# Performance work log

Measured on AMD Instinct MI355X. Metric: run time of the kernel, lower is better.

The kernel has to match this reference:

```python
import jax, jax.numpy as jnp
import numpy as np


def _igd(x, pf):
    # pf: [M, d] reference front, x: [N, d] candidate set
    # squared Euclidean distances via ||a||^2 + ||b||^2 - 2 a.b (cdist expansion)
    pf_sq = jnp.sum(pf * pf, axis=1, keepdims=True)          # [M, 1]
    x_sq = jnp.sum(x * x, axis=1, keepdims=True).T            # [1, N]
    cross = pf @ x.T                                          # [M, N]
    d2 = jnp.maximum(pf_sq + x_sq - 2.0 * cross, 0.0)
    dist = jnp.sqrt(d2)                                       # [M, N]
    # IGD: mean over reference points of min distance to candidate set
    return jnp.mean(jnp.min(dist, axis=1))


def setup_inputs() -> dict:
    key = jax.random.key(0)
    k1, k2 = jax.random.split(key)
    N, M, D = 16384, 16384, 64
    x = jax.random.normal(k1, (N, D), dtype=jnp.float32)
    pf = jax.random.normal(k2, (M, D), dtype=jnp.float32)
    return {"x": x, "pf": pf}


def reference(x, pf):
    return _igd(x, pf)
```

## Files before the change

kernel.cpp:

```cpp
#include <hip/hip_runtime.h>


typedef float f32x16 __attribute__((ext_vector_type(16)));
typedef int i32x8 __attribute__((ext_vector_type(8)));
typedef unsigned long long u64;

#define DIM 64
#define NSPLIT 12
#define UNITB 2048
#define CHUNKU 8
#define CHUNKB (CHUNKU * UNITB)
#define MTILE 256

union BFrag { u64 q[4]; i32x8 v; };

__device__ inline unsigned char enc_e4m3(float f) {
    unsigned int u = __float_as_uint(f);
    unsigned int s = (u >> 24) & 0x80u;
    unsigned int a = u & 0x7FFFFFFFu;
    if ((a >> 23) >= 121u) {
        unsigned int lsb = (a >> 20) & 1u;
        unsigned int r = a + 0x7FFFFu + lsb;
        int e = (int)(r >> 23) - 120;
        unsigned int m = (r >> 20) & 7u;
        if (e > 15 || (e == 15 && m == 7u)) return (unsigned char)(s | 0x7Eu);
        return (unsigned char)(s | ((unsigned)e << 3) | m);
    }
    int m = (int)rintf(__uint_as_float(a) * 512.0f);
    return (unsigned char)(s | (unsigned)m);
}

__device__ inline float dec_e4m3(unsigned char b) {
    int e = (b >> 3) & 15, m = b & 7;
    float v = e ? __uint_as_float((unsigned)((e + 120) << 23) | ((unsigned)m << 20))
                : (float)m * 0.001953125f;
    return (b & 0x80) ? -v : v;
}

__global__ void pack_kernel(const float* __restrict__ x, const float* __restrict__ pf,
                            unsigned char* __restrict__ Bp, unsigned char* __restrict__ Ab,
                            float* __restrict__ xsq, float* __restrict__ pfsq,
                            float* __restrict__ out, int N, int M) {
    int gid = blockIdx.x * blockDim.x + threadIdx.x;
    if (gid == 0) out[0] = 0.f;
    if (gid < N * 4) {
        int col = gid >> 2, t = gid & 3;
        const float* s = x + (size_t)col * DIM + t * 16;
        float partial = 0.f;
        u64 w[2] = {0, 0};
#pragma unroll
        for (int h = 0; h < 2; ++h) {
            float4 v0 = *(const float4*)(s + h * 8);
            float4 v1 = *(const float4*)(s + h * 8 + 4);
            float f[8] = {v0.x, v0.y, v0.z, v0.w, v1.x, v1.y, v1.z, v1.w};
#pragma unroll
            for (int j = 0; j < 8; ++j) {
                unsigned char b = enc_e4m3(f[j]);
                w[h] |= (u64)b << (8 * j);
                float d = dec_e4m3(b);
                partial += d * d;
            }
        }
        int u = col >> 5, c31 = col & 31;
        unsigned char* ub = Bp + (size_t)u * UNITB;
        int h = t >> 1;
#pragma unroll
        for (int ss = 0; ss < 2; ++ss) {
            int q = (t & 1) * 2 + ss;
            *(u64*)(ub + (size_t)q * 512 + (size_t)(h * 32 + c31) * 8) = w[ss];
        }
        partial += __shfl_xor(partial, 1);
        partial += __shfl_xor(partial, 2);
        if (t == 0) xsq[col] = partial;
    } else {
        int g = gid - N * 4;
        int row = g >> 2, q = g & 3;
        if (row >= M) return;
        const float* s = pf + (size_t)row * DIM + q * 16;
        float partial = 0.f;
        u64 w[2] = {0, 0};
#pragma unroll
        for (int h = 0; h < 2; ++h) {
            float4 v0 = *(const float4*)(s + h * 8);
            float4 v1 = *(const float4*)(s + h * 8 + 4);
            float f[8] = {v0.x, v0.y, v0.z, v0.w, v1.x, v1.y, v1.z, v1.w};
#pragma unroll
            for (int j = 0; j < 8; ++j) {
                unsigned char b = enc_e4m3(f[j] * -2.f);
                w[h] |= (u64)b << (8 * j);
                float d = dec_e4m3(b);
                partial += d * d;
            }
        }
        *(u64*)(Ab + (size_t)row * DIM + q * 16)     = w[0];
        *(u64*)(Ab + (size_t)row * DIM + q * 16 + 8) = w[1];
        partial += __shfl_xor(partial, 1);
        partial += __shfl_xor(partial, 2);
        if (q == 0) pfsq[row] = partial * 0.25f;
    }
}

__global__ __launch_bounds__(256, 3)
void igd_main(const unsigned char* __restrict__ A, const unsigned char* __restrict__ Bp,
              const float* __restrict__ xsq, float* __restrict__ partial, int N) {
    __shared__ unsigned char ldsB[2][CHUNKB];
    __shared__ float ldsX[2][CHUNKU * 32];
    const int tid = threadIdx.x;
    const int mTile  = blockIdx.x;
    const int nsplit = blockIdx.y;
    const int lane = tid & 63;
    const int wave = tid >> 6;
    const int half = lane >> 5;
    const int l31  = lane & 31;
    const int rowBase = mTile * MTILE + wave * 64;

    const int utotal = N / 32;
    const int ubase  = utotal / NSPLIT;
    const int urem   = utotal % NSPLIT;
    const int ustart = nsplit * ubase + (nsplit < urem ? nsplit : urem);
    const int ucount = ubase + (nsplit < urem ? 1 : 0);
    const int nch = (ucount + CHUNKU - 1) / CHUNKU;

    BFrag a[2];
#pragma unroll
    for (int g = 0; g < 2; ++g) {
        const unsigned char* ap = A + (size_t)(rowBase + 32 * g + l31) * DIM + half * 32;
#pragma unroll
        for (int qq = 0; qq < 4; ++qq)
            a[g].q[qq] = *(const u64*)(ap + qq * 8);
    }

    const unsigned char* gB = Bp + (size_t)ustart * UNITB;
    const float* gX = xsq + ustart * 32;

#define STAGE(c, buf)                                                          \
    {                                                                          \
        int bytes = (ucount - (c) * CHUNKU) < CHUNKU ? (ucount - (c) * CHUNKU) * UNITB : CHUNKB; \
        const unsigned char* src = gB + (size_t)(c) * CHUNKB;                  \
        _Pragma("unroll")                                                      \
        for (int i = 0; i < 4; ++i) {                                          \
            int off = i * 4096 + tid * 16;                                     \
            if (off < bytes)                                                   \
                *(float4*)(&ldsB[buf][off]) = *(const float4*)(src + off);     \
        }                                                                      \
        int xcnt = bytes >> 6;                                                 \
        if (tid < xcnt) ldsX[buf][tid] = gX[(c) * (CHUNKU * 32) + tid];        \
    }

    f32x16 zero, m0, m1;
#pragma unroll
    for (int r = 0; r < 16; ++r) { zero[r] = 0.f; m0[r] = 1e30f; m1[r] = 1e30f; }

    BFrag b0, b1;

#define LOADF(rr, lb, u)                                                       \
    {                                                                          \
        const unsigned char* p = (lb) + (u) * UNITB;                           \
        rr.q[0] = *(const u64*)(p);                                            \
        rr.q[1] = *(const u64*)(p + 512);                                      \
        rr.q[2] = *(const u64*)(p + 1024);                                     \
        rr.q[3] = *(const u64*)(p + 1536);                                     \
    }

#define COMPUTE(rr, xq)                                                        \
    {                                                                          \
        f32x16 acc0 = __builtin_amdgcn_mfma_scale_f32_32x32x64_f8f6f4(         \
            a[0].v, rr.v, zero, 0, 0, 0, 0x7F7F7F7F, 0, 0x7F7F7F7F);           \
        f32x16 acc1 = __builtin_amdgcn_mfma_scale_f32_32x32x64_f8f6f4(         \
            a[1].v, rr.v, zero, 0, 0, 0, 0x7F7F7F7F, 0, 0x7F7F7F7F);           \
        _Pragma("unroll")                                                      \
        for (int r = 0; r < 16; ++r) {                                         \
            m0[r] = fminf(m0[r], acc0[r] + (xq));                              \
            m1[r] = fminf(m1[r], acc1[r] + (xq));                              \
        }                                                                      \
    }

    STAGE(0, 0);
    __syncthreads();

    for (int c = 0; c < nch; ++c) {
        const int buf = c & 1;
        if (c + 1 < nch) STAGE(c + 1, buf ^ 1);
        const int cnt = (ucount - c * CHUNKU) < CHUNKU ? (ucount - c * CHUNKU) : CHUNKU;
        const unsigned char* lb = &ldsB[buf][0] + lane * 8;
        const float* lx = &ldsX[buf][0] + l31;
        if (cnt == CHUNKU) {
            LOADF(b0, lb, 0);
#pragma unroll
            for (int u = 0; u < CHUNKU; u += 2) {
                LOADF(b1, lb, u + 1);
                COMPUTE(b0, lx[u * 32]);
                if (u + 2 < CHUNKU) LOADF(b0, lb, u + 2);
                COMPUTE(b1, lx[(u + 1) * 32]);
            }
        } else {
            for (int u = 0; u < cnt; ++u) {
                LOADF(b0, lb, u);
                COMPUTE(b0, lx[u * 32]);
            }
        }
        __syncthreads();
    }
#undef STAGE
#undef LOADF
#undef COMPUTE

#pragma unroll
    for (int mask = 1; mask <= 16; mask <<= 1) {
#pragma unroll
        for (int r = 0; r < 16; ++r) {
            m0[r] = fminf(m0[r], __shfl_xor(m0[r], mask));
            m1[r] = fminf(m1[r], __shfl_xor(m1[r], mask));
        }
    }
    if (l31 == 0) {
#pragma unroll
        for (int r = 0; r < 16; ++r) {
            int row0 = rowBase + (r & 3) + 8 * (r >> 2) + 4 * half;
            partial[(size_t)row0 * NSPLIT + nsplit] = m0[r];
            partial[(size_t)(row0 + 32) * NSPLIT + nsplit] = m1[r];
        }
    }
}

__global__ void reduce_kernel(const float* __restrict__ partial, const float* __restrict__ pfsq,
                              float* __restrict__ out, int M, float invM) {
    int row = blockIdx.x * blockDim.x + threadIdx.x;
    float v = 0.f;
    if (row < M) {
        const float* p = partial + (size_t)row * NSPLIT;
        float mn = 3.4e38f;
#pragma unroll
        for (int s = 0; s < NSPLIT; ++s) mn = fminf(mn, p[s]);
        float d2 = mn + pfsq[row];
        v = sqrtf(fmaxf(d2, 0.f)) * invM;
    }
#pragma unroll
    for (int m = 1; m < 64; m <<= 1) v += __shfl_xor(v, m);
    __shared__ float wsum[4];
    int lane = threadIdx.x & 63, w = threadIdx.x >> 6;
    if (lane == 0) wsum[w] = v;
    __syncthreads();
    if (threadIdx.x == 0) atomicAdd(out, wsum[0] + wsum[1] + wsum[2] + wsum[3]);
}

extern "C" void kernel_launch(void* const* d_in, const int* in_sizes, int n_in,
                              void* d_out, int out_size, void* d_ws, size_t ws_size,
                              hipStream_t stream) {
    const float* x  = (const float*)d_in[0];
    const float* pf = (const float*)d_in[1];
    const int N = in_sizes[0] / DIM;
    const int M = in_sizes[1] / DIM;

    char* ws = (char*)d_ws;
    unsigned char* Bp = (unsigned char*)ws;
    unsigned char* Ab = (unsigned char*)(ws + (size_t)N * DIM);
    float* xsq  = (float*)(ws + (size_t)(N + M) * DIM);
    float* pfsq = xsq + N;
    float* part = pfsq + M;

    int packThreads = (N + M) * 4;
    pack_kernel<<<dim3((packThreads + 255) / 256), 256, 0, stream>>>(
        x, pf, Bp, Ab, xsq, pfsq, (float*)d_out, N, M);
    igd_main<<<dim3(M / MTILE, NSPLIT), 256, 0, stream>>>(Ab, Bp, xsq, part, N);
    reduce_kernel<<<dim3((M + 255) / 256), 256, 0, stream>>>(part, pfsq, (float*)d_out, M, 1.f / (float)M);
}
```

Baseline: 92.31 us.

## Load whole per-block B slice into LDS via direct global-to-LDS loads

Doubles the N-split so each block handles at most 22 units, then loads its entire B slice and x-norms into LDS at once with global_load_lds. This replaces the double-buffered chunk loop and its per-chunk barriers with a single barrier and a flat compute loop. It adds grid blocks and partial-min traffic for the reduce kernel. The larger LDS footprint (~45KB) may limit occupancy, and the global-load latency is no longer overlapped with compute inside a block.

```diff
diff --git a/kernel.cpp b/kernel.cpp
--- a/kernel.cpp
+++ b/kernel.cpp
@@ -6,13 +6,23 @@
 typedef unsigned long long u64;
 
 #define DIM 64
-#define NSPLIT 12
+#define NSPLIT 24
 #define UNITB 2048
-#define CHUNKU 8
-#define CHUNKB (CHUNKU * UNITB)
+#define MAXU 22
 #define MTILE 256
 
 union BFrag { u64 q[4]; i32x8 v; };
+
+__device__ __forceinline__ void g2lds16(const void* g, void* l) {
+    __builtin_amdgcn_global_load_lds(
+        (const __attribute__((address_space(1))) unsigned int*)g,
+        (__attribute__((address_space(3))) unsigned int*)l, 16, 0, 0);
+}
+__device__ __forceinline__ void g2lds4(const void* g, void* l) {
+    __builtin_amdgcn_global_load_lds(
+        (const __attribute__((address_space(1))) unsigned int*)g,
+        (__attribute__((address_space(3))) unsigned int*)l, 4, 0, 0);
+}
 
 __device__ inline unsigned char enc_e4m3(float f) {
     unsigned int u = __float_as_uint(f);
@@ -103,8 +113,8 @@
 __global__ __launch_bounds__(256, 3)
 void igd_main(const unsigned char* __restrict__ A, const unsigned char* __restrict__ Bp,
               const float* __restrict__ xsq, float* __restrict__ partial, int N) {
-    __shared__ unsigned char ldsB[2][CHUNKB];
-    __shared__ float ldsX[2][CHUNKU * 32];
+    __shared__ unsigned char ldsB[MAXU * UNITB];
+    __shared__ float ldsX[MAXU * 32];
     const int tid = threadIdx.x;
     const int mTile  = blockIdx.x;
     const int nsplit = blockIdx.y;
@@ -119,7 +129,24 @@
     const int urem   = utotal % NSPLIT;
     const int ustart = nsplit * ubase + (nsplit < urem ? nsplit : urem);
     const int ucount = ubase + (nsplit < urem ? 1 : 0);
-    const int nch = (ucount + CHUNKU - 1) / CHUNKU;
+
+    const unsigned char* gB = Bp + (size_t)ustart * UNITB;
+    const float* gX = xsq + ustart * 32;
+
+    {
+        int bytes = ucount * UNITB;
+#pragma unroll
+        for (int i = 0; i < 11; ++i) {
+            int off = i * 4096 + tid * 16;
+            if (off < bytes) g2lds16(gB + off, &ldsB[off]);
+        }
+        int xcnt = ucount * 32;
+#pragma unroll
+        for (int j = 0; j < 3; ++j) {
+            int idx = j * 256 + tid;
+            if (idx < xcnt) g2lds4(gX + idx, &ldsX[idx]);
+        }
+    }
 
     BFrag a[2];
 #pragma unroll
@@ -130,44 +157,27 @@
             a[g].q[qq] = *(const u64*)(ap + qq * 8);
     }
 
-    const unsigned char* gB = Bp + (size_t)ustart * UNITB;
-    const float* gX = xsq + ustart * 32;
-
-#define STAGE(c, buf)                                                          \
+    f32x16 zero, m0, m1;
+#pragma unroll
+    for (int r = 0; r < 16; ++r) { zero[r] = 0.f; m0[r] = 1e30f; m1[r] = 1e30f; }
+
+    __syncthreads();
+
+#define LOADF(rr, u)                                                           \
     {                                                                          \
-        int bytes = (ucount - (c) * CHUNKU) < CHUNKU ? (ucount - (c) * CHUNKU) * UNITB : CHUNKB; \
-        const unsigned char* src = gB + (size_t)(c) * CHUNKB;                  \
-        _Pragma("unroll")                                                      \
-        for (int i = 0; i < 4; ++i) {                                          \
-            int off = i * 4096 + tid * 16;                                     \
-            if (off < bytes)                                                   \
-                *(float4*)(&ldsB[buf][off]) = *(const float4*)(src + off);     \
-        }                                                                      \
-        int xcnt = bytes >> 6;                                                 \
-        if (tid < xcnt) ldsX[buf][tid] = gX[(c) * (CHUNKU * 32) + tid];        \
-    }
-
-    f32x16 zero, m0, m1;
-#pragma unroll
-    for (int r = 0; r < 16; ++r) { zero[r] = 0.f; m0[r] = 1e30f; m1[r] = 1e30f; }
-
-    BFrag b0, b1;
-
-#define LOADF(rr, lb, u)                                                       \
-    {                                                                          \
-        const unsigned char* p = (lb) + (u) * UNITB;                           \
+        const unsigned char* p = &ldsB[0] + lane * 8 + (u) * UNITB;            \
         rr.q[0] = *(const u64*)(p);                                            \
         rr.q[1] = *(const u64*)(p + 512);                                      \
         rr.q[2] = *(const u64*)(p + 1024);                                     \
         rr.q[3] = *(const u64*)(p + 1536);                                     \
     }
 
-#define COMPUTE(rr, xq)                                                        \
+#define STEP(bfrag, xq)                                                        \
     {                                                                          \
         f32x16 acc0 = __builtin_amdgcn_mfma_scale_f32_32x32x64_f8f6f4(         \
-            a[0].v, rr.v, zero, 0, 0, 0, 0x7F7F7F7F, 0, 0x7F7F7F7F);           \
+            a[0].v, bfrag.v, zero, 0, 0, 0, 0x7F7F7F7F, 0, 0x7F7F7F7F);        \
         f32x16 acc1 = __builtin_amdgcn_mfma_scale_f32_32x32x64_f8f6f4(         \
-            a[1].v, rr.v, zero, 0, 0, 0, 0x7F7F7F7F, 0, 0x7F7F7F7F);           \
+            a[1].v, bfrag.v, zero, 0, 0, 0, 0x7F7F7F7F, 0, 0x7F7F7F7F);        \
         _Pragma("unroll")                                                      \
         for (int r = 0; r < 16; ++r) {                                         \
             m0[r] = fminf(m0[r], acc0[r] + (xq));                              \
@@ -175,35 +185,18 @@
         }                                                                      \
     }
 
-    STAGE(0, 0);
-    __syncthreads();
-
-    for (int c = 0; c < nch; ++c) {
-        const int buf = c & 1;
-        if (c + 1 < nch) STAGE(c + 1, buf ^ 1);
-        const int cnt = (ucount - c * CHUNKU) < CHUNKU ? (ucount - c * CHUNKU) : CHUNKU;
-        const unsigned char* lb = &ldsB[buf][0] + lane * 8;
-        const float* lx = &ldsX[buf][0] + l31;
-        if (cnt == CHUNKU) {
-            LOADF(b0, lb, 0);
-#pragma unroll
-            for (int u = 0; u < CHUNKU; u += 2) {
-                LOADF(b1, lb, u + 1);
-                COMPUTE(b0, lx[u * 32]);
-                if (u + 2 < CHUNKU) LOADF(b0, lb, u + 2);
-                COMPUTE(b1, lx[(u + 1) * 32]);
-            }
-        } else {
-            for (int u = 0; u < cnt; ++u) {
-                LOADF(b0, lb, u);
-                COMPUTE(b0, lx[u * 32]);
-            }
-        }
-        __syncthreads();
-    }
-#undef STAGE
+    {
+        BFrag b0, b1;
+        LOADF(b0, 0);
+        for (int u = 0; u < ucount; u += 2) {
+            if (u + 1 < ucount) LOADF(b1, u + 1);
+            STEP(b0, ldsX[u * 32 + l31]);
+            if (u + 2 < ucount) LOADF(b0, u + 2);
+            if (u + 1 < ucount) STEP(b1, ldsX[(u + 1) * 32 + l31]);
+        }
+    }
 #undef LOADF
-#undef COMPUTE
+#undef STEP
 
 #pragma unroll
     for (int mask = 1; mask <= 16; mask <<= 1) {
@@ -230,7 +223,7 @@
     if (row < M) {
         const float* p = partial + (size_t)row * NSPLIT;
         float mn = 3.4e38f;
-#pragma unroll
+#pragma unroll 8
         for (int s = 0; s < NSPLIT; ++s) mn = fminf(mn, p[s]);
         float d2 = mn + pfsq[row];
         v = sqrtf(fmaxf(d2, 0.f)) * invM;
```

New measurement: 101.0 us. 9.4% more time.
